# Kernel tuning notes

Measured on AMD Instinct MI355X. Metric: run time of the kernel, lower is better.

## Reference

```python
import jax, jax.numpy as jnp
import numpy as np

B, N, C, H, BS = 4, 4096, 1024, 16, 64
E = C // H          # head dim = 64
EPS = 1e-3

def setup_inputs() -> dict:
    key = jax.random.key(0)
    k0, k1, k2, k3 = jax.random.split(key, 4)
    x = jax.random.normal(k0, (B, N, C), jnp.float32)
    qkv_w = jax.random.normal(k1, (3 * C, C), jnp.float32) * 0.02
    proj_w = jax.random.normal(k2, (C, C), jnp.float32) * 0.02
    proj_b = jax.random.normal(k3, (C,), jnp.float32) * 0.02
    return {"x": x, "qkv_w": qkv_w, "proj_w": proj_w, "proj_b": proj_b}

def reference(x, qkv_w, proj_w, proj_b):
    b, n, c = x.shape
    h, e, bs = H, E, BS
    u = n // bs  # number of buckets
    # qkv projection (no bias), split to (B,H,N,e) per q/k/v
    qkv = (x @ qkv_w.T).reshape(b, n, 3, h, e).transpose(2, 0, 3, 1, 4)
    q, k, v = qkv[0], qkv[1], qkv[2]
    # feature maps: softmax(q) scaled, exp(k)
    q = jax.nn.softmax(q, axis=-1) * (e ** -0.5)
    k = jnp.exp(k)
    # bucket along sequence: (B,H,U,BS,e)
    b_q = q.reshape(b, h, u, bs, e)
    b_k = k.reshape(b, h, u, bs, e)
    b_v = v.reshape(b, h, u, bs, e)
    # per-bucket k sums and inter-bucket cumulative sums
    b_k_cumsum = jnp.cumsum(b_k.sum(axis=-2), axis=-2)            # (B,H,U,e)
    context = jnp.einsum('bhund,bhune->bhude', b_k, b_v)          # (B,H,U,e,e)
    context = jnp.cumsum(context, axis=2)
    # exclusive shift by one bucket (bucket_size > 1 path in original)
    context = jnp.concatenate(
        [jnp.zeros_like(context[:, :, :1]), context[:, :, :-1]], axis=2)
    b_k_cumsum = jnp.concatenate(
        [jnp.zeros_like(b_k_cumsum[:, :, :1]), b_k_cumsum[:, :, :-1]], axis=2)
    # normalizer, clamped from below at eps
    D_inv = 1.0 / jnp.maximum(
        jnp.einsum('bhud,bhund->bhun', b_k_cumsum, b_q), EPS)
    attn = jnp.einsum('bhund,bhude,bhun->bhune', b_q, context, D_inv)
    out = attn.reshape(b, h, n, e).transpose(0, 2, 1, 3).reshape(b, n, c)
    # output projection (dropouts are identity at eval)
    return out @ proj_w.T + proj_b
```

## Files before the change

kernel.cpp:

```cpp
#include <hip/hip_runtime.h>
#include <stdint.h>


typedef unsigned short u16;
typedef unsigned int u32;
typedef u16   u16x4  __attribute__((ext_vector_type(4)));
typedef u16   u16x8  __attribute__((ext_vector_type(8)));
typedef float f32x4  __attribute__((ext_vector_type(4)));
typedef float float4v __attribute__((ext_vector_type(4)));
typedef __bf16 bf16x8 __attribute__((ext_vector_type(8)));

__device__ __forceinline__ u16 f2bf(float f) {
  return __builtin_bit_cast(u16, (__bf16)f);
}
__device__ __forceinline__ float bf2f(u16 h) {
  return (float)__builtin_bit_cast(__bf16, h);
}

__device__ __forceinline__ void stage16(const u16* g, u16* l) {
  __builtin_amdgcn_global_load_lds(
      (const __attribute__((address_space(1))) u32*)g,
      (__attribute__((address_space(3))) u32*)l, 16, 0, 0);
}

__global__ __launch_bounds__(256) void cvt_all(
    const float* __restrict__ x, const float* __restrict__ wqf,
    const float* __restrict__ wpf, u16* __restrict__ xb,
    u16* __restrict__ wq, u16* __restrict__ wp) {
  int i = blockIdx.x * 256 + threadIdx.x;
  const float* in; u16* out; int j;
  if (i < 4194304)      { in = x;   out = xb; j = i; }
  else if (i < 4980736) { in = wqf; out = wq; j = i - 4194304; }
  else                  { in = wpf; out = wp; j = i - 4980736; }
  float4v v = reinterpret_cast<const float4v*>(in)[j];
  u16x4 o;
  o.x = f2bf(v.x); o.y = f2bf(v.y); o.z = f2bf(v.z); o.w = f2bf(v.w);
  reinterpret_cast<u16x4*>(out)[j] = o;
}

template <int EPI>
__global__ __launch_bounds__(512, 2) void gemm256(
    const u16* __restrict__ A,
    const u16* __restrict__ B,
    const float* __restrict__ bias,
    float* __restrict__ Cf,
    u16* __restrict__ Qf, u16* __restrict__ Kt, u16* __restrict__ Vt,
    float* __restrict__ ksum,
    int N, int K, int NT) {
  __shared__ u16 As[2][2][256][32];
  __shared__ u16 Bs[2][2][256][32];
  const int tid = threadIdx.x, lane = tid & 63, wave = tid >> 6;
  const int wm = wave >> 2, wn = wave & 3;
  const int l15 = lane & 15, l4 = lane >> 4;
  const int ntn = N >> 8;
  const int cpx = gridDim.x >> 3;
  const int bid = (blockIdx.x & 7) * cpx + (blockIdx.x >> 3);
  const int bm = bid / ntn, bn = bid % ntn;

  const int srow = tid >> 2;
  const int gsl8 = ((tid & 3) ^ ((tid >> 3) & 3)) * 8;
  const u16* Ag = A + (size_t)(bm * 256 + srow) * K + gsl8;
  const u16* Bg = B + (size_t)(bn * 256 + srow) * K + gsl8;
  const size_t rj = (size_t)128 * K;
  const int slotr = (l4 ^ ((l15 >> 1) & 3)) * 8;

  f32x4 acc[8][4] = {};
  bf16x8 a0, a1, a2, a3, a4, a5, a6, a7, b0, b1, b2, b3;

#define STG(P, buf, kh, kt)                                        \
  { const u16* g_ = P##g + (kt) + (kh) * 32;                       \
    stage16(g_,      &P##s[buf][kh][wave * 16][0]);                \
    stage16(g_ + rj, &P##s[buf][kh][128 + wave * 16][0]); }

#define LDA(r0_, r1_, r2_, r3_, kk, mh)                                  \
  { const u16* p_ = &As[cur][kk][wm * 128 + (mh) * 64 + l15][0] + slotr; \
    r0_ = *(const bf16x8*)(p_);                                          \
    r1_ = *(const bf16x8*)(p_ + 512);                                    \
    r2_ = *(const bf16x8*)(p_ + 1024);                                   \
    r3_ = *(const bf16x8*)(p_ + 1536); }

#define LDB(kk)                                                    \
  { const u16* p_ = &Bs[cur][kk][wn * 64 + l15][0] + slotr;        \
    b0 = *(const bf16x8*)(p_);                                     \
    b1 = *(const bf16x8*)(p_ + 512);                               \
    b2 = *(const bf16x8*)(p_ + 1024);                              \
    b3 = *(const bf16x8*)(p_ + 1536); }

#define MM(x, y, z) z = __builtin_amdgcn_mfma_f32_16x16x32_bf16(x, y, z, 0, 0, 0)
#define MFMA16(mb, x0, x1, x2, x3)                                 \
  __builtin_amdgcn_s_setprio(1);                                   \
  MM(x0, b0, acc[(mb) + 0][0]); MM(x0, b1, acc[(mb) + 0][1]);      \
  MM(x0, b2, acc[(mb) + 0][2]); MM(x0, b3, acc[(mb) + 0][3]);      \
  MM(x1, b0, acc[(mb) + 1][0]); MM(x1, b1, acc[(mb) + 1][1]);      \
  MM(x1, b2, acc[(mb) + 1][2]); MM(x1, b3, acc[(mb) + 1][3]);      \
  MM(x2, b0, acc[(mb) + 2][0]); MM(x2, b1, acc[(mb) + 2][1]);      \
  MM(x2, b2, acc[(mb) + 2][2]); MM(x2, b3, acc[(mb) + 2][3]);      \
  MM(x3, b0, acc[(mb) + 3][0]); MM(x3, b1, acc[(mb) + 3][1]);      \
  MM(x3, b2, acc[(mb) + 3][2]); MM(x3, b3, acc[(mb) + 3][3]);      \
  __builtin_amdgcn_s_setprio(0);

#define BARF()                                                     \
  { asm volatile("" ::: "memory");                                 \
    __builtin_amdgcn_s_barrier();                                  \
    asm volatile("" ::: "memory"); }

  STG(A, 0, 0, 0) STG(B, 0, 0, 0) STG(A, 0, 1, 0) STG(B, 0, 1, 0)
  asm volatile("s_waitcnt vmcnt(0)" ::: "memory");
  __builtin_amdgcn_s_barrier();
  asm volatile("" ::: "memory");

  for (int t = 0; t < NT; ++t) {
    const int cur = t & 1, nxt = cur ^ 1;
    const int ktn = (t + 1) << 6;
    const bool pre = (t + 1 < NT);
    LDB(0)
    LDA(a0, a1, a2, a3, 0, 0)
    LDA(a4, a5, a6, a7, 0, 1)
    if (pre) STG(A, nxt, 0, ktn)
    MFMA16(0, a0, a1, a2, a3)
    if (pre) STG(B, nxt, 0, ktn)
    MFMA16(4, a4, a5, a6, a7)
    if (pre) { asm volatile("s_waitcnt vmcnt(4)" ::: "memory"); }
    else     { asm volatile("s_waitcnt vmcnt(0)" ::: "memory"); }
    BARF()
    LDB(1)
    LDA(a0, a1, a2, a3, 1, 0)
    LDA(a4, a5, a6, a7, 1, 1)
    if (pre) STG(A, nxt, 1, ktn)
    MFMA16(0, a0, a1, a2, a3)
    if (pre) STG(B, nxt, 1, ktn)
    MFMA16(4, a4, a5, a6, a7)
    if (pre) { asm volatile("s_waitcnt vmcnt(4)" ::: "memory"); }
    BARF()
  }
#undef STG
#undef LDA
#undef LDB
#undef MM
#undef MFMA16
#undef BARF

  const int row0 = bm * 256 + wm * 128 + l4 * 4;
  const int col0 = bn * 256 + wn * 64 + l15;
  if constexpr (EPI == 0) {
    float bv[4];
#pragma unroll
    for (int ni = 0; ni < 4; ++ni) bv[ni] = bias[col0 + ni * 16];
#pragma unroll
    for (int mi = 0; mi < 8; ++mi)
#pragma unroll
      for (int i = 0; i < 4; ++i) {
        size_t r = (size_t)(row0 + mi * 16 + i) * N;
#pragma unroll
        for (int ni = 0; ni < 4; ++ni)
          Cf[r + col0 + ni * 16] = acc[mi][ni][i] + bv[ni];
      }
  } else {
    const int i3 = bn >> 2;
    const int h  = ((bn & 3) << 2) + wn;
    if (i3 == 0) {
#pragma unroll
      for (int mi = 0; mi < 8; ++mi)
#pragma unroll
        for (int i = 0; i < 4; ++i) {
          const int row = row0 + mi * 16 + i;
          const int bb = row >> 12, uu = (row >> 6) & 63, nn = row & 63;
          u16* op = Qf + ((size_t)((bb * 16 + h) * 64 + uu)) * 4096
                        + nn * 64 + l15;
          float v0 = acc[mi][0][i], v1 = acc[mi][1][i];
          float v2 = acc[mi][2][i], v3 = acc[mi][3][i];
          float mx = fmaxf(fmaxf(v0, v1), fmaxf(v2, v3));
          mx = fmaxf(mx, __shfl_xor(mx, 1));
          mx = fmaxf(mx, __shfl_xor(mx, 2));
          mx = fmaxf(mx, __shfl_xor(mx, 4));
          mx = fmaxf(mx, __shfl_xor(mx, 8));
          float e0 = __expf(v0 - mx), e1 = __expf(v1 - mx);
          float e2 = __expf(v2 - mx), e3 = __expf(v3 - mx);
          float s = e0 + e1 + e2 + e3;
          s += __shfl_xor(s, 1); s += __shfl_xor(s, 2);
          s += __shfl_xor(s, 4); s += __shfl_xor(s, 8);
          float inv = 0.125f / s;
          op[0]  = f2bf(e0 * inv); op[16] = f2bf(e1 * inv);
          op[32] = f2bf(e2 * inv); op[48] = f2bf(e3 * inv);
        }
    } else if (i3 == 1) {
      float sk0[4] = {0.f, 0.f, 0.f, 0.f};
      float sk1[4] = {0.f, 0.f, 0.f, 0.f};
#pragma unroll
      for (int mi = 0; mi < 8; ++mi) {
        const int row = row0 + mi * 16;
        const int bb = row >> 12, uu = (row >> 6) & 63, nn = row & 63;
        u16* op = Kt + ((size_t)((bb * 16 + h) * 64 + uu)) * 4096 + nn;
#pragma unroll
        for (int ni = 0; ni < 4; ++ni) {
          float e0 = __expf(acc[mi][ni][0]);
          float e1 = __expf(acc[mi][ni][1]);
          float e2 = __expf(acc[mi][ni][2]);
          float e3 = __expf(acc[mi][ni][3]);
          u16x4 o;
          o.x = f2bf(e0); o.y = f2bf(e1); o.z = f2bf(e2); o.w = f2bf(e3);
          *reinterpret_cast<u16x4*>(op + (ni * 16 + l15) * 64) = o;
          if (mi < 4) sk0[ni] += e0 + e1 + e2 + e3;
          else        sk1[ni] += e0 + e1 + e2 + e3;
        }
      }
#pragma unroll
      for (int ni = 0; ni < 4; ++ni) {
        sk0[ni] += __shfl_xor(sk0[ni], 16); sk0[ni] += __shfl_xor(sk0[ni], 32);
        sk1[ni] += __shfl_xor(sk1[ni], 16); sk1[ni] += __shfl_xor(sk1[ni], 32);
      }
      if (lane < 16) {
        const int nb0 = bm * 256 + wm * 128;
        const size_t bkt0 = (size_t)(((nb0 >> 12) * 16 + h) * 64 + ((nb0 >> 6) & 63));
#pragma unroll
        for (int ni = 0; ni < 4; ++ni) {
          ksum[bkt0 * 64 + ni * 16 + l15]       = sk0[ni];
          ksum[(bkt0 + 1) * 64 + ni * 16 + l15] = sk1[ni];
        }
      }
    } else {
#pragma unroll
      for (int mi = 0; mi < 8; ++mi) {
        const int row = row0 + mi * 16;
        const int bb = row >> 12, uu = (row >> 6) & 63, nn = row & 63;
        u16* op = Vt + ((size_t)((bb * 16 + h) * 64 + uu)) * 4096 + nn;
#pragma unroll
        for (int ni = 0; ni < 4; ++ni) {
          u16x4 o;
          o.x = f2bf(acc[mi][ni][0]); o.y = f2bf(acc[mi][ni][1]);
          o.z = f2bf(acc[mi][ni][2]); o.w = f2bf(acc[mi][ni][3]);
          *reinterpret_cast<u16x4*>(op + (ni * 16 + l15) * 64) = o;
        }
      }
    }
  }
}

__global__ __launch_bounds__(256) void scanctx2(
    const u16* __restrict__ Kt,
    const u16* __restrict__ Vt,
    u16* __restrict__ ctxb) {
  const int bh = blockIdx.x >> 2, ec = blockIdx.x & 3;
  const int tid = threadIdx.x, lane = tid & 63, wave = tid >> 6;
  const int l15 = lane & 15, l4 = lane >> 4;
  __shared__ u16 KtL[2][2][64][72];
  __shared__ u16 VtL[2][2][16][72];

  const size_t bbase = (size_t)bh * 64 * 4096;
  const int kr0 = tid >> 3, ks = (tid & 7) * 8;
  const int kr1 = 32 + kr0;
  const bool dov = tid < 128;
  const int vr = tid >> 3, vs = (tid & 7) * 8;

  f32x4 acc = {0.f, 0.f, 0.f, 0.f};
  u16x8 ka0, ka1, kb0, kb1, va = {}, vb = {};

#define GLD(u_, kx0, kx1, vx)                                          \
  { const size_t nb = bbase + (size_t)(u_) * 4096;                     \
    kx0 = *reinterpret_cast<const u16x8*>(Kt + nb + kr0 * 64 + ks);    \
    kx1 = *reinterpret_cast<const u16x8*>(Kt + nb + kr1 * 64 + ks);    \
    if (dov) vx = *reinterpret_cast<const u16x8*>(                     \
        Vt + nb + (ec * 16 + vr) * 64 + vs); }
#define LWR(buf, j, kx0, kx1, vx)                                      \
  { *reinterpret_cast<u16x8*>(&KtL[buf][j][kr0][ks]) = kx0;            \
    *reinterpret_cast<u16x8*>(&KtL[buf][j][kr1][ks]) = kx1;            \
    if (dov) *reinterpret_cast<u16x8*>(&VtL[buf][j][vr][vs]) = vx; }
#define ACC(buf, j)                                                    \
  _Pragma("unroll")                                                    \
  for (int kk = 0; kk < 2; ++kk) {                                     \
    bf16x8 av = *reinterpret_cast<const bf16x8*>(                      \
        &VtL[buf][j][l15][kk * 32 + l4 * 8]);                          \
    bf16x8 bk = *reinterpret_cast<const bf16x8*>(                      \
        &KtL[buf][j][wave * 16 + l15][kk * 32 + l4 * 8]);              \
    acc = __builtin_amdgcn_mfma_f32_16x16x32_bf16(av, bk, acc, 0, 0, 0); }

  GLD(0, ka0, ka1, va) GLD(1, kb0, kb1, vb)
  LWR(0, 0, ka0, ka1, va) LWR(0, 1, kb0, kb1, vb)
  __syncthreads();

  for (int u = 0; u < 64; u += 2) {
    const int cur = (u >> 1) & 1, nxt = cur ^ 1;
    const bool pre = (u + 2 < 64);
    if (pre) { GLD(u + 2, ka0, ka1, va) GLD(u + 3, kb0, kb1, vb) }
    u16* cb0 = ctxb + bbase + (size_t)u * 4096 + wave * 16 + l15;
#pragma unroll
    for (int i = 0; i < 4; ++i) cb0[(ec * 16 + l4 * 4 + i) * 64] = f2bf(acc[i]);
    ACC(cur, 0)
    u16* cb1 = cb0 + 4096;
#pragma unroll
    for (int i = 0; i < 4; ++i) cb1[(ec * 16 + l4 * 4 + i) * 64] = f2bf(acc[i]);
    ACC(cur, 1)
    if (pre) { LWR(nxt, 0, ka0, ka1, va) LWR(nxt, 1, kb0, kb1, vb) }
    __syncthreads();
  }
#undef GLD
#undef LWR
#undef ACC
}

__global__ __launch_bounds__(64) void scanK(float* __restrict__ ksum) {
  const int bh = blockIdx.x;
  float* p = ksum + (size_t)bh * 4096 + threadIdx.x;
  float run = 0.f;
#define LK(i) p[(size_t)(i) * 64]
  float c0 = LK(0), c1 = LK(1), c2 = LK(2), c3 = LK(3);
  for (int u = 0; u < 64; u += 4) {
    const int i4 = u + 4 < 64 ? u + 4 : 63, i5 = u + 5 < 64 ? u + 5 : 63;
    const int i6 = u + 6 < 64 ? u + 6 : 63, i7 = u + 7 < 64 ? u + 7 : 63;
    float n0 = LK(i4), n1 = LK(i5), n2 = LK(i6), n3 = LK(i7);
    LK(u) = run;     run += c0;
    LK(u + 1) = run; run += c1;
    LK(u + 2) = run; run += c2;
    LK(u + 3) = run; run += c3;
    c0 = n0; c1 = n1; c2 = n2; c3 = n3;
  }
#undef LK
}

__global__ __launch_bounds__(256) void apply(
    const u16* __restrict__ Q, const u16* __restrict__ ctxc,
    const float* __restrict__ kcum, u16* __restrict__ AT) {
  const int bid = blockIdx.x;
  const int u = bid & 63, bh = bid >> 6, b = bh >> 4, h = bh & 15;
  const int tid = threadIdx.x, lane = tid & 63, wave = tid >> 6;
  const int l15 = lane & 15, l4 = lane >> 4;
  __shared__ float kc[64];

  const size_t base = (size_t)bid * 4096;
  if (tid < 64) kc[tid] = kcum[(size_t)bid * 64 + tid];
  __syncthreads();

  bf16x8 aq[2];
  float dpart = 0.f;
#pragma unroll
  for (int kk = 0; kk < 2; ++kk) {
    aq[kk] = *reinterpret_cast<const bf16x8*>(
        Q + base + (wave * 16 + l15) * 64 + kk * 32 + l4 * 8);
    const float* kcp = &kc[kk * 32 + l4 * 8];
#pragma unroll
    for (int j = 0; j < 8; ++j) dpart += (float)aq[kk][j] * kcp[j];
  }
  dpart += __shfl_xor(dpart, 16);
  dpart += __shfl_xor(dpart, 32);
  const float dinv_self = 1.f / fmaxf(dpart, 1e-3f);
  float dv[4];
#pragma unroll
  for (int i = 0; i < 4; ++i) dv[i] = __shfl(dinv_self, l4 * 4 + i);

  f32x4 acc[4] = {};
  const u16* Cu = ctxc + base;
#pragma unroll
  for (int kk = 0; kk < 2; ++kk)
#pragma unroll
    for (int ni = 0; ni < 4; ++ni) {
      bf16x8 bc = *reinterpret_cast<const bf16x8*>(
          Cu + (ni * 16 + l15) * 64 + kk * 32 + l4 * 8);
      acc[ni] = __builtin_amdgcn_mfma_f32_16x16x32_bf16(aq[kk], bc, acc[ni], 0, 0, 0);
    }
  const size_t orow = ((size_t)b * 4096 + u * 64 + wave * 16 + l4 * 4) * 1024 + h * 64;
#pragma unroll
  for (int i = 0; i < 4; ++i) {
#pragma unroll
    for (int ni = 0; ni < 4; ++ni)
      AT[orow + (size_t)i * 1024 + ni * 16 + l15] = f2bf(acc[ni][i] * dv[i]);
  }
}

extern "C" void kernel_launch(void* const* d_in, const int* in_sizes, int n_in,
                              void* d_out, int out_size, void* d_ws, size_t ws_size,
                              hipStream_t stream) {
  (void)in_sizes; (void)n_in; (void)out_size; (void)ws_size;
  const float* x      = (const float*)d_in[0];
  const float* qkv_w  = (const float*)d_in[1];
  const float* proj_w = (const float*)d_in[2];
  const float* proj_b = (const float*)d_in[3];
  float* out = (float*)d_out;

  char* ws = (char*)d_ws;
  u16* xb    = (u16*)(ws);
  u16* wq    = (u16*)(ws + 33554432);
  u16* wp    = (u16*)(ws + 39845888);
  u16* Qf    = (u16*)(ws + 41943040);
  u16* Kt    = (u16*)(ws + 75497472);
  u16* Vt    = (u16*)(ws + 109051904);
  u16* ctxb  = (u16*)(ws + 142606336);
  float* ksum = (float*)(ws + 176160768);
  u16* AT    = Kt;

  cvt_all<<<dim3(20480), dim3(256), 0, stream>>>(x, qkv_w, proj_w, xb, wq, wp);

  gemm256<2><<<dim3(64 * 12), dim3(512), 0, stream>>>(
      xb, wq, nullptr, nullptr, Qf, Kt, Vt, ksum, 3072, 1024, 16);
  scanK<<<dim3(64), dim3(64), 0, stream>>>(ksum);
  scanctx2<<<dim3(256), dim3(256), 0, stream>>>(Kt, Vt, ctxb);
  apply<<<dim3(4096), dim3(256), 0, stream>>>(Qf, ctxb, ksum, AT);
  gemm256<0><<<dim3(64 * 4), dim3(512), 0, stream>>>(
      AT, wp, proj_b, out, nullptr, nullptr, nullptr, nullptr, 1024, 1024, 16);
}
```

Measured before the change: 234.3 us.

## Fuse fp32-to-bf16 conversion of x into the QKV GEMM A-tile loads

Removes the separate conversion pass over the activation x and instead loads fp32 x directly in the QKV GEMM, converting to bf16 in registers before writing the LDS tile. Only the weights are still converted in a standalone kernel. This removes an extra full read/write of the large activation tensor, but the GEMM now reads twice as many bytes for A, holds extra registers for the prefetched fp32 data, and uses a restructured wait/barrier schedule that may reduce overlap.

```diff
diff --git a/kernel.cpp b/kernel.cpp
--- a/kernel.cpp
+++ b/kernel.cpp
@@ -23,15 +23,13 @@
       (__attribute__((address_space(3))) u32*)l, 16, 0, 0);
 }
 
-__global__ __launch_bounds__(256) void cvt_all(
-    const float* __restrict__ x, const float* __restrict__ wqf,
-    const float* __restrict__ wpf, u16* __restrict__ xb,
+__global__ __launch_bounds__(256) void cvt_w(
+    const float* __restrict__ wqf, const float* __restrict__ wpf,
     u16* __restrict__ wq, u16* __restrict__ wp) {
   int i = blockIdx.x * 256 + threadIdx.x;
   const float* in; u16* out; int j;
-  if (i < 4194304)      { in = x;   out = xb; j = i; }
-  else if (i < 4980736) { in = wqf; out = wq; j = i - 4194304; }
-  else                  { in = wpf; out = wp; j = i - 4980736; }
+  if (i < 786432) { in = wqf; out = wq; j = i; }
+  else            { in = wpf; out = wp; j = i - 786432; }
   float4v v = reinterpret_cast<const float4v*>(in)[j];
   u16x4 o;
   o.x = f2bf(v.x); o.y = f2bf(v.y); o.z = f2bf(v.z); o.w = f2bf(v.w);
@@ -41,6 +39,7 @@
 template <int EPI>
 __global__ __launch_bounds__(512, 2) void gemm256(
     const u16* __restrict__ A,
+    const float* __restrict__ Xf,
     const u16* __restrict__ B,
     const float* __restrict__ bias,
     float* __restrict__ Cf,
@@ -59,18 +58,41 @@
 
   const int srow = tid >> 2;
   const int gsl8 = ((tid & 3) ^ ((tid >> 3) & 3)) * 8;
-  const u16* Ag = A + (size_t)(bm * 256 + srow) * K + gsl8;
+  const u16* Ag = A ? A + (size_t)(bm * 256 + srow) * K + gsl8 : nullptr;
+  const float* Xg = Xf ? Xf + (size_t)(bm * 256 + srow) * K + gsl8 : nullptr;
   const u16* Bg = B + (size_t)(bn * 256 + srow) * K + gsl8;
   const size_t rj = (size_t)128 * K;
   const int slotr = (l4 ^ ((l15 >> 1) & 3)) * 8;
 
   f32x4 acc[8][4] = {};
   bf16x8 a0, a1, a2, a3, a4, a5, a6, a7, b0, b1, b2, b3;
-
-#define STG(P, buf, kh, kt)                                        \
-  { const u16* g_ = P##g + (kt) + (kh) * 32;                       \
-    stage16(g_,      &P##s[buf][kh][wave * 16][0]);                \
-    stage16(g_ + rj, &P##s[buf][kh][128 + wave * 16][0]); }
+  float4v p0, p1, p2, p3, p4, p5, p6, p7;
+
+#define STGA(buf, kh, kt)                                          \
+  { const u16* g_ = Ag + (kt) + (kh) * 32;                         \
+    stage16(g_,      &As[buf][kh][wave * 16][0]);                  \
+    stage16(g_ + rj, &As[buf][kh][128 + wave * 16][0]); }
+#define STGB(buf, kh, kt)                                          \
+  { const u16* g_ = Bg + (kt) + (kh) * 32;                         \
+    stage16(g_,      &Bs[buf][kh][wave * 16][0]);                  \
+    stage16(g_ + rj, &Bs[buf][kh][128 + wave * 16][0]); }
+
+#define AFLD(kh, kt, q0, q1, q2, q3)                               \
+  { const float* g0 = Xg + (kt) + (kh) * 32;                       \
+    q0 = *(const float4v*)(g0); q1 = *(const float4v*)(g0 + 4);    \
+    const float* g1 = g0 + rj;                                     \
+    q2 = *(const float4v*)(g1); q3 = *(const float4v*)(g1 + 4); }
+#define AWR(buf, kh, q0, q1, q2, q3)                               \
+  { u16x8 w;                                                       \
+    w[0] = f2bf(q0.x); w[1] = f2bf(q0.y); w[2] = f2bf(q0.z);       \
+    w[3] = f2bf(q0.w); w[4] = f2bf(q1.x); w[5] = f2bf(q1.y);       \
+    w[6] = f2bf(q1.z); w[7] = f2bf(q1.w);                          \
+    *(u16x8*)(&As[buf][kh][srow][(tid & 3) * 8]) = w;              \
+    u16x8 w2;                                                      \
+    w2[0] = f2bf(q2.x); w2[1] = f2bf(q2.y); w2[2] = f2bf(q2.z);    \
+    w2[3] = f2bf(q2.w); w2[4] = f2bf(q3.x); w2[5] = f2bf(q3.y);    \
+    w2[6] = f2bf(q3.z); w2[7] = f2bf(q3.w);                        \
+    *(u16x8*)(&As[buf][kh][128 + srow][(tid & 3) * 8]) = w2; }
 
 #define LDA(r0_, r1_, r2_, r3_, kk, mh)                                  \
   { const u16* p_ = &As[cur][kk][wm * 128 + (mh) * 64 + l15][0] + slotr; \
@@ -104,8 +126,16 @@
     __builtin_amdgcn_s_barrier();                                  \
     asm volatile("" ::: "memory"); }
 
-  STG(A, 0, 0, 0) STG(B, 0, 0, 0) STG(A, 0, 1, 0) STG(B, 0, 1, 0)
-  asm volatile("s_waitcnt vmcnt(0)" ::: "memory");
+  if constexpr (EPI == 2) {
+    AFLD(0, 0, p0, p1, p2, p3) AFLD(1, 0, p4, p5, p6, p7)
+    STGB(0, 0, 0) STGB(0, 1, 0)
+    asm volatile("s_waitcnt vmcnt(4)" ::: "memory");
+    AWR(0, 0, p0, p1, p2, p3) AWR(0, 1, p4, p5, p6, p7)
+    asm volatile("s_waitcnt vmcnt(0) lgkmcnt(0)" ::: "memory");
+  } else {
+    STGA(0, 0, 0) STGB(0, 0, 0) STGA(0, 1, 0) STGB(0, 1, 0)
+    asm volatile("s_waitcnt vmcnt(0)" ::: "memory");
+  }
   __builtin_amdgcn_s_barrier();
   asm volatile("" ::: "memory");
 
@@ -113,27 +143,56 @@
     const int cur = t & 1, nxt = cur ^ 1;
     const int ktn = (t + 1) << 6;
     const bool pre = (t + 1 < NT);
-    LDB(0)
-    LDA(a0, a1, a2, a3, 0, 0)
-    LDA(a4, a5, a6, a7, 0, 1)
-    if (pre) STG(A, nxt, 0, ktn)
-    MFMA16(0, a0, a1, a2, a3)
-    if (pre) STG(B, nxt, 0, ktn)
-    MFMA16(4, a4, a5, a6, a7)
-    if (pre) { asm volatile("s_waitcnt vmcnt(4)" ::: "memory"); }
-    else     { asm volatile("s_waitcnt vmcnt(0)" ::: "memory"); }
-    BARF()
-    LDB(1)
-    LDA(a0, a1, a2, a3, 1, 0)
-    LDA(a4, a5, a6, a7, 1, 1)
-    if (pre) STG(A, nxt, 1, ktn)
-    MFMA16(0, a0, a1, a2, a3)
-    if (pre) STG(B, nxt, 1, ktn)
-    MFMA16(4, a4, a5, a6, a7)
-    if (pre) { asm volatile("s_waitcnt vmcnt(4)" ::: "memory"); }
-    BARF()
-  }
-#undef STG
+    if constexpr (EPI == 2) {
+      LDB(0)
+      LDA(a0, a1, a2, a3, 0, 0)
+      LDA(a4, a5, a6, a7, 0, 1)
+      if (pre) {
+        AFLD(0, ktn, p0, p1, p2, p3) AFLD(1, ktn, p4, p5, p6, p7)
+        STGB(nxt, 0, ktn) STGB(nxt, 1, ktn)
+      }
+      MFMA16(0, a0, a1, a2, a3)
+      MFMA16(4, a4, a5, a6, a7)
+      if (pre) { asm volatile("s_waitcnt vmcnt(12)" ::: "memory"); }
+      else     { asm volatile("s_waitcnt vmcnt(0)" ::: "memory"); }
+      BARF()
+      LDB(1)
+      LDA(a0, a1, a2, a3, 1, 0)
+      LDA(a4, a5, a6, a7, 1, 1)
+      MFMA16(0, a0, a1, a2, a3)
+      MFMA16(4, a4, a5, a6, a7)
+      if (pre) {
+        asm volatile("s_waitcnt vmcnt(4)" ::: "memory");
+        AWR(nxt, 0, p0, p1, p2, p3) AWR(nxt, 1, p4, p5, p6, p7)
+        asm volatile("s_waitcnt vmcnt(2) lgkmcnt(0)" ::: "memory");
+        BARF()
+      }
+    } else {
+      LDB(0)
+      LDA(a0, a1, a2, a3, 0, 0)
+      LDA(a4, a5, a6, a7, 0, 1)
+      if (pre) STGA(nxt, 0, ktn)
+      MFMA16(0, a0, a1, a2, a3)
+      if (pre) STGB(nxt, 0, ktn)
+      MFMA16(4, a4, a5, a6, a7)
+      if (pre) { asm volatile("s_waitcnt vmcnt(4)" ::: "memory"); }
+      else     { asm volatile("s_waitcnt vmcnt(0)" ::: "memory"); }
+      BARF()
+      LDB(1)
+      LDA(a0, a1, a2, a3, 1, 0)
+      LDA(a4, a5, a6, a7, 1, 1)
+      if (pre) STGA(nxt, 1, ktn)
+      MFMA16(0, a0, a1, a2, a3)
+      if (pre) STGB(nxt, 1, ktn)
+      MFMA16(4, a4, a5, a6, a7)
+      if (pre) { asm volatile("s_waitcnt vmcnt(4)" ::: "memory"); }
+      BARF()
+    }
+  }
+#undef STGA
+#undef STGB
+#undef AFLD
+#undef AWR
 #undef LDA
 #undef LDB
 #undef MM
@@ -377,7 +436,6 @@
   float* out = (float*)d_out;
 
   char* ws = (char*)d_ws;
-  u16* xb    = (u16*)(ws);
   u16* wq    = (u16*)(ws + 33554432);
   u16* wp    = (u16*)(ws + 39845888);
   u16* Qf    = (u16*)(ws + 41943040);
@@ -387,13 +445,14 @@
   float* ksum = (float*)(ws + 176160768);
   u16* AT    = Kt;
 
-  cvt_all<<<dim3(20480), dim3(256), 0, stream>>>(x, qkv_w, proj_w, xb, wq, wp);
+  cvt_w<<<dim3(4096), dim3(256), 0, stream>>>(qkv_w, proj_w, wq, wp);
 
   gemm256<2><<<dim3(64 * 12), dim3(512), 0, stream>>>(
-      xb, wq, nullptr, nullptr, Qf, Kt, Vt, ksum, 3072, 1024, 16);
+      nullptr, x, wq, nullptr, nullptr, Qf, Kt, Vt, ksum, 3072, 1024, 16);
   scanK<<<dim3(64), dim3(64), 0, stream>>>(ksum);
   scanctx2<<<dim3(256), dim3(256), 0, stream>>>(Kt, Vt, ctxb);
   apply<<<dim3(4096), dim3(256), 0, stream>>>(Qf, ctxb, ksum, AT);
   gemm256<0><<<dim3(64 * 4), dim3(512), 0, stream>>>(
-      AT, wp, proj_b, out, nullptr, nullptr, nullptr, nullptr, 1024, 1024, 16);
-}
+      AT, nullptr, wp, proj_b, out, nullptr, nullptr, nullptr, nullptr,
+      1024, 1024, 16);
+}
```

Measured after the change: 259.2 us. +10.6%, slower.
